# Kernel tuning notes

Measured on AMD Instinct MI355X. Metric: run time of the kernel, lower is better.

## Reference

```python
import jax, jax.numpy as jnp
import numpy as np
import math

B, S, D, H_HEADS, K_SPAN = 2, 2048, 64, 12, 512  # batch, seq, head dim, heads, pos_ebd_size


def setup_inputs() -> dict:
    key = jax.random.key(0)
    ks = jax.random.split(key, 12)
    init = lambda k, shp: (jax.random.normal(k, shp, dtype=jnp.float32) * 0.02)
    H = jax.random.normal(ks[0], (B, S, D), dtype=jnp.float32)
    pos_embeddings = jax.random.normal(ks[1], (2 * K_SPAN, D), dtype=jnp.float32)
    # classic DeBERTa relative positions: i - j (2-D, as required by the torch code path)
    idx = jnp.arange(S)
    relative_pos = (idx[:, None] - idx[None, :]).astype(jnp.int64)
    OH = H_HEADS * D
    return {
        "H": H,
        "pos_embeddings": pos_embeddings,
        "relative_pos": relative_pos,
        "Wq": init(ks[2], (OH, D)), "bq": jnp.zeros((OH,), jnp.float32),
        "Wk": init(ks[3], (OH, D)), "bk": jnp.zeros((OH,), jnp.float32),
        "Wv": init(ks[4], (OH, D)), "bv": jnp.zeros((OH,), jnp.float32),
        "Wpq": init(ks[5], (OH, D)), "bpq": jnp.zeros((OH,), jnp.float32),
        "Wpk": init(ks[6], (OH, D)), "bpk": jnp.zeros((OH,), jnp.float32),
    }


def _heads(x):
    # [..., S, h*d] -> [..., h, S, d]
    b, s, _ = x.shape
    return x.reshape(b, s, H_HEADS, D).transpose(0, 2, 1, 3)


def reference(H, pos_embeddings, relative_pos, Wq, bq, Wk, bk, Wv, bv, Wpq, bpq, Wpk, bpk):
    proj = lambda x, W, b: x @ W.T + b
    q = _heads(proj(H, Wq, bq))  # [B,h,S,d]
    k = _heads(proj(H, Wk, bk))
    v = _heads(proj(H, Wv, bv))

    # content-to-content scores
    scores = jnp.einsum('bhqd,bhkd->bhqk', q, k)  # [B,h,S,S]

    # relative position projections over the full 2K span
    pk = proj(pos_embeddings, Wpk, bpk).reshape(2 * K_SPAN, H_HEADS, D).transpose(1, 0, 2)  # [h,2K,d]
    pq = proj(pos_embeddings, Wpq, bpq).reshape(2 * K_SPAN, H_HEADS, D).transpose(1, 0, 2)

    rel = relative_pos.astype(jnp.int32)
    # content-to-position: gather over 2K axis with clamped (i-j)+K
    c2p = jnp.einsum('bhqd,hrd->bhqr', q, pk)  # [B,h,S,2K]
    c2p_pos = jnp.clip(rel + K_SPAN, 0, 2 * K_SPAN - 1)  # [S,S]
    c2p_idx = jnp.broadcast_to(c2p_pos[None, None], (B, H_HEADS, S, S))
    c2p_att = jnp.take_along_axis(c2p, c2p_idx, axis=-1)  # [B,h,S,S]

    # position-to-content: gather over 2K axis with clamped -(i-j)+K, then transpose
    p2c = jnp.einsum('bhkd,hrd->bhkr', k, pq)  # [B,h,S,2K]
    p2c_pos = jnp.clip(-rel + K_SPAN, 0, 2 * K_SPAN - 1)
    p2c_idx = jnp.broadcast_to(p2c_pos[None, None], (B, H_HEADS, S, S))
    p2c_att = jnp.take_along_axis(p2c, p2c_idx, axis=-1).swapaxes(-1, -2)  # [B,h,S,S]

    scores = (scores + c2p_att + p2c_att) / math.sqrt(D * 3)
    probs = jax.nn.softmax(scores, axis=-1)
    ctx = jnp.einsum('bhqk,bhkd->bhqd', probs, v)  # [B,h,S,d]
    return ctx.transpose(0, 2, 1, 3).reshape(B, S, H_HEADS * D)
```

## Files before the change

kernel.cpp:

```cpp
#include <hip/hip_runtime.h>
#include <math.h>


#define S_LEN 2048
#define NH    12
#define TWOK  1024
#define QSZ   3145728
#define PSZ   786432
#define POSF  11010048

typedef __bf16 bf16x8 __attribute__((ext_vector_type(8)));
typedef unsigned short u16x8 __attribute__((ext_vector_type(8)));
typedef unsigned short u16x4 __attribute__((ext_vector_type(4)));
typedef float f32x4  __attribute__((ext_vector_type(4)));
typedef float f32x16 __attribute__((ext_vector_type(16)));
typedef unsigned int u32x4 __attribute__((ext_vector_type(4)));

__device__ __forceinline__ unsigned short f2bf(float f) {
  return __builtin_bit_cast(unsigned short, (__bf16)f);
}
__device__ __forceinline__ unsigned pk2bf(float a, float b) {
  return ((unsigned)__builtin_bit_cast(unsigned short, (__bf16)b) << 16)
       | (unsigned)__builtin_bit_cast(unsigned short, (__bf16)a);
}
__device__ __forceinline__ float bf2f(unsigned short h) {
  return __builtin_bit_cast(float, ((unsigned)h) << 16);
}
__device__ __forceinline__ bf16x8 ld_bf8(const unsigned short* p) {
  return __builtin_bit_cast(bf16x8, *(const u16x8*)p);
}

__global__ __launch_bounds__(256) void prep_kernel(
    const float* __restrict__ Hx, const float* __restrict__ pos,
    const float* __restrict__ Wq, const float* __restrict__ Wk,
    const float* __restrict__ Wv, const float* __restrict__ Wpk,
    const float* __restrict__ Wpq,
    const float* __restrict__ bq, const float* __restrict__ bk,
    const float* __restrict__ bv, const float* __restrict__ bpk,
    const float* __restrict__ bpq,
    unsigned short* __restrict__ whi, unsigned short* __restrict__ wlo,
    unsigned short* __restrict__ wall, float* __restrict__ ball) {
  int t0 = blockIdx.x * 256 + threadIdx.x;
  for (int pass = 0; pass < 8; ++pass) {
    int idx = t0 + pass * 73728;
    if (idx < 327680) {
      float v = (idx < 262144) ? Hx[idx] : pos[idx - 262144];
      __bf16 hi = (__bf16)v;
      float lo = v - (float)hi;
      whi[idx] = __builtin_bit_cast(unsigned short, hi);
      wlo[idx] = f2bf(lo);
    } else if (idx < 573440) {
      int k = idx - 327680;
      int mat = k / 49152, off = k - mat * 49152;
      const float* W = mat==0?Wq: mat==1?Wk: mat==2?Wv: mat==3?Wpk:Wpq;
      wall[k] = f2bf(W[off]);
    } else if (idx < 577280) {
      int k = idx - 573440;
      int mat = k / 768, off = k - mat * 768;
      const float* B = mat==0?bq: mat==1?bk: mat==2?bv: mat==3?bpk:bpq;
      ball[k] = B[off];
    }
  }
}

__global__ __launch_bounds__(256) void proj_gemm(
    const unsigned short* __restrict__ whi, const unsigned short* __restrict__ wlo,
    const unsigned short* __restrict__ wall, const float* __restrict__ ball,
    unsigned short* __restrict__ ws) {
  unsigned short* qg  = ws;
  unsigned short* kg  = ws + QSZ;
  unsigned short* vtg = ws + 2 * QSZ;
  unsigned short* pkg = ws + 3 * QSZ;
  unsigned short* pqg = ws + 3 * QSZ + PSZ;

  int tid = threadIdx.x, w = tid >> 6, l = tid & 63, lg = l >> 4, lr = l & 15;

  for (int tt = 0; tt < 4; ++tt) {
    int tile = blockIdx.x * 4 + tt;
    int rbase, obase, wrow, isA;
    if (tile < 2304) { rbase = (tile / 36) * 64;        obase = (tile % 36) * 64; wrow = obase;        isA = 1; }
    else { int b2 = tile - 2304; rbase = 4096 + (b2 / 24) * 64; obase = (b2 % 24) * 64; wrow = 2304 + obase; isA = 0; }

    int mat = obase / 768;
    int h = (obase % 768) >> 6;
    int ohrow = wrow + w * 16;

    bf16x8 wf[2];
    #pragma unroll
    for (int ks = 0; ks < 2; ++ks)
      wf[ks] = ld_bf8(wall + (ohrow + lr) * 64 + ks * 32 + 8 * lg);

    if (isA && mat == 2) {
      float bias = ball[ohrow + lr];
      int d = w * 16 + lr;
      #pragma unroll
      for (int tg = 0; tg < 4; ++tg) {
        f32x4 acc = {0.f, 0.f, 0.f, 0.f};
        #pragma unroll
        for (int ks = 0; ks < 2; ++ks) {
          bf16x8 xh = ld_bf8(whi + (rbase + tg * 16 + lr) * 64 + ks * 32 + 8 * lg);
          bf16x8 xl = ld_bf8(wlo + (rbase + tg * 16 + lr) * 64 + ks * 32 + 8 * lg);
          acc = __builtin_amdgcn_mfma_f32_16x16x32_bf16(xh, wf[ks], acc, 0, 0, 0);
          acc = __builtin_amdgcn_mfma_f32_16x16x32_bf16(xl, wf[ks], acc, 0, 0, 0);
        }
        int tok0 = rbase + tg * 16 + 4 * lg;
        int bb = tok0 >> 11, i0 = tok0 & 2047, bh = bb * NH + h;
        u16x4 pv;
        #pragma unroll
        for (int e = 0; e < 4; ++e) pv[e] = f2bf(acc[e] + bias);
        *(u16x4*)(vtg + (size_t)(bh * 64 + d) * S_LEN + i0) = pv;
      }
    } else {
      float4 bias4 = *(const float4*)(ball + ohrow + 4 * lg);
      int d0 = w * 16 + 4 * lg;
      #pragma unroll
      for (int tg = 0; tg < 4; ++tg) {
        f32x4 acc = {0.f, 0.f, 0.f, 0.f};
        #pragma unroll
        for (int ks = 0; ks < 2; ++ks) {
          bf16x8 xh = ld_bf8(whi + (rbase + tg * 16 + lr) * 64 + ks * 32 + 8 * lg);
          bf16x8 xl = ld_bf8(wlo + (rbase + tg * 16 + lr) * 64 + ks * 32 + 8 * lg);
          acc = __builtin_amdgcn_mfma_f32_16x16x32_bf16(wf[ks], xh, acc, 0, 0, 0);
          acc = __builtin_amdgcn_mfma_f32_16x16x32_bf16(wf[ks], xl, acc, 0, 0, 0);
        }
        int tok = rbase + tg * 16 + lr;
        u16x4 pv;
        pv[0] = f2bf(acc[0] + bias4.x); pv[1] = f2bf(acc[1] + bias4.y);
        pv[2] = f2bf(acc[2] + bias4.z); pv[3] = f2bf(acc[3] + bias4.w);
        if (isA) {
          int bb = tok >> 11, i = tok & 2047, bh = bb * NH + h;
          unsigned short* dst = (mat == 0 ? qg : kg) + (size_t)(bh * S_LEN + i) * 64 + d0;
          *(u16x4*)dst = pv;
        } else {
          int prow = tok - 4096;
          unsigned short* dst = (mat == 0 ? pkg : pqg) + (size_t)(h * TWOK + prow) * 64 + d0;
          *(u16x4*)dst = pv;
        }
      }
    }
  }
}

__global__ __launch_bounds__(256) void pos_dots(
    const unsigned short* __restrict__ ws, float* __restrict__ c2p0,
    float* __restrict__ c2p1023, float* __restrict__ p2c0,
    float* __restrict__ p2c1023) {
  int t0 = blockIdx.x * 256 + threadIdx.x;
  for (int pass = 0; pass < 4; ++pass) {
    int t = t0 + pass * 24576;
    int isK = t >= 49152;
    int row = isK ? t - 49152 : t;
    int h = (row >> 11) % NH;
    const unsigned short* src = ws + (isK ? QSZ : 0) + row * 64;
    const unsigned short* pA = ws + 3 * QSZ + (isK ? PSZ : 0) + (h * TWOK) * 64;
    const unsigned short* pB = pA + 1023 * 64;
    float a0 = 0.f, a1 = 0.f;
    #pragma unroll
    for (int c = 0; c < 8; ++c) {
      u16x8 xv = *(const u16x8*)(src + c * 8);
      u16x8 av = *(const u16x8*)(pA + c * 8);
      u16x8 bv = *(const u16x8*)(pB + c * 8);
      #pragma unroll
      for (int e = 0; e < 8; ++e) {
        float x = bf2f(xv[e]);
        a0 += x * bf2f(av[e]);
        a1 += x * bf2f(bv[e]);
      }
    }
    if (isK) { p2c0[row] = a0; p2c1023[row] = a1; }
    else     { c2p0[row] = a0; c2p1023[row] = a1; }
  }
}

template<int SPLIT>
__global__ __launch_bounds__(512, 2) void attn_kernel(
    const unsigned short* __restrict__ ws, float* __restrict__ out,
    unsigned short* __restrict__ ctxP, float* __restrict__ mlP) {
  const unsigned short* qg  = ws;
  const unsigned short* kg  = ws + QSZ;
  const unsigned short* vtg = ws + 2 * QSZ;
  const unsigned short* pkg = ws + 3 * QSZ;
  const unsigned short* pqg = ws + 3 * QSZ + PSZ;
  const float* c2p0g    = (const float*)(ws + POSF);
  const float* c2p1023g = c2p0g + 49152;
  const float* p2c0g    = c2p0g + 98304;
  const float* p2c1023g = c2p0g + 147456;

  __shared__ __align__(16) unsigned int tbl2all[8 * 2048];
  unsigned int* tbl2 = tbl2all + (threadIdx.x >> 6) * 2048;

  const int bid = blockIdx.x;
  const int g = bid & 7;
  const int wid = threadIdx.x >> 6;
  const int u = (bid >> 3) * 8 + wid;
  const int sk = u & (SPLIT - 1);
  const int v = u / SPLIT;
  const int bh = 8 * (v % 3) + g;
  const int it32 = v / 3;
  const int b = bh / NH, h = bh - b * NH;
  const int l = threadIdx.x & 63;
  const int iL = l & 31, h5 = l >> 5;
  const int i0w = it32 * 32;
  const int ig = i0w + iL;

  const unsigned short* qb  = qg  + bh * (S_LEN * 64);
  const unsigned short* kb  = kg  + bh * (S_LEN * 64);
  const unsigned short* vb  = vtg + bh * (64 * S_LEN);
  const unsigned short* pkb = pkg + h * (TWOK * 64);
  const unsigned short* pqb = pqg + h * (TWOK * 64);

  const float CS = 1.4426950408889634f / sqrtf(192.0f);

  bf16x8 qf[4];
  #pragma unroll
  for (int kc = 0; kc < 4; ++kc)
    qf[kc] = ld_bf8(qb + ig * 64 + kc * 16 + 8 * h5);

  const float c2pLO = c2p0g[bh * S_LEN + ig];
  const float c2pHI = c2p1023g[bh * S_LEN + ig];

  f32x16 ctx0 = 0.f, ctx1 = 0.f;
  float m_ = -1e30f, l_ = 0.f;

  for (int t = 0; t < 32 / SPLIT; ++t) {
    const int jt = sk + t * SPLIT;
    const int j0 = jt * 64;
    const int D0w = 512 + i0w - j0;
    const int rlo = D0w - 63;
    const int rhi = rlo + 94;

    bf16x8 kf0[4], kf1[4];
    #pragma unroll
    for (int kc = 0; kc < 4; ++kc) {
      kf0[kc] = ld_bf8(kb + (j0 + iL) * 64 + kc * 16 + 8 * h5);
      kf1[kc] = ld_bf8(kb + (j0 + 32 + iL) * 64 + kc * 16 + 8 * h5);
    }
    bf16x8 vf0[4], vf1[4];
    #pragma unroll
    for (int kc = 0; kc < 4; ++kc) {
      vf0[kc] = ld_bf8(vb + (iL) * S_LEN + j0 + kc * 16 + 8 * h5);
      vf1[kc] = ld_bf8(vb + (32 + iL) * S_LEN + j0 + kc * 16 + 8 * h5);
    }

    f32x16 s0 = 0.f, s1 = 0.f;
    #pragma unroll
    for (int kc = 0; kc < 4; ++kc) {
      s0 = __builtin_amdgcn_mfma_f32_32x32x16_bf16(kf0[kc], qf[kc], s0, 0, 0, 0);
      s1 = __builtin_amdgcn_mfma_f32_32x32x16_bf16(kf1[kc], qf[kc], s1, 0, 0, 0);
    }

    if (rlo >= 1023) {
      float pa = p2c1023g[bh * S_LEN + j0 + iL];
      float pb = p2c1023g[bh * S_LEN + j0 + 32 + iL];
      #pragma unroll
      for (int rr = 0; rr < 16; ++rr) {
        const int j32 = (rr & 3) + 8 * (rr >> 2) + 4 * h5;
        s0[rr] = (s0[rr] + c2pHI + __shfl(pa, j32)) * CS;
        s1[rr] = (s1[rr] + c2pHI + __shfl(pb, j32)) * CS;
      }
    } else if (rhi <= 0) {
      float pa = p2c0g[bh * S_LEN + j0 + iL];
      float pb = p2c0g[bh * S_LEN + j0 + 32 + iL];
      #pragma unroll
      for (int rr = 0; rr < 16; ++rr) {
        const int j32 = (rr & 3) + 8 * (rr >> 2) + 4 * h5;
        s0[rr] = (s0[rr] + c2pLO + __shfl(pa, j32)) * CS;
        s1[rr] = (s1[rr] + c2pLO + __shfl(pb, j32)) * CS;
      }
    } else {
      const int rminc = rlo < 0 ? 0 : rlo;
      const int rmaxc = rhi > 1023 ? 1023 : rhi;
      const int bstart = rminc > 928 ? 928 : rminc;
      const int nbands = ((rmaxc - bstart) >> 5) + 1;
      const int base = D0w - bstart;
      const int interior = (rlo >= 0) & (rhi <= 1023);

      for (int nb = 0; nb < nbands; ++nb) {
        const int relb0 = nb * 32;
        const bool needC  = (relb0 <= base + 31) && (relb0 + 31 >= base - 63);
        const bool needP0 = (relb0 <= base + 31) && (relb0 + 31 >= base - 31);
        const bool needP1 = (relb0 <= base - 1)  && (relb0 + 31 >= base - 63);
        const int rrow = bstart + relb0 + iL;

        if (needC) {
          f32x16 ac = 0.f;
          #pragma unroll
          for (int kc = 0; kc < 4; ++kc) {
            bf16x8 fk = ld_bf8(pkb + rrow * 64 + kc * 16 + 8 * h5);
            ac = __builtin_amdgcn_mfma_f32_32x32x16_bf16(fk, qf[kc], ac, 0, 0, 0);
          }
          #pragma unroll
          for (int q4 = 0; q4 < 4; ++q4) {
            #pragma unroll
            for (int e = 0; e < 4; ++e) {
              const int relb = relb0 + 8 * q4 + 4 * h5 + e;
              const int js = base + iL - relb;
              if (js >= 0 && js < 64)
                ((unsigned short*)tbl2)[(js * 32 + iL) * 2] = f2bf(ac[4 * q4 + e]);
            }
          }
        }
        if (needP0 | needP1) {
          f32x16 a0 = 0.f, a1 = 0.f;
          #pragma unroll
          for (int kc = 0; kc < 4; ++kc) {
            bf16x8 fq = ld_bf8(pqb + rrow * 64 + kc * 16 + 8 * h5);
            if (needP0) a0 = __builtin_amdgcn_mfma_f32_32x32x16_bf16(fq, kf0[kc], a0, 0, 0, 0);
            if (needP1) a1 = __builtin_amdgcn_mfma_f32_32x32x16_bf16(fq, kf1[kc], a1, 0, 0, 0);
          }
          #pragma unroll
          for (int q4 = 0; q4 < 4; ++q4) {
            #pragma unroll
            for (int e = 0; e < 4; ++e) {
              const int relb = relb0 + 8 * q4 + 4 * h5 + e;
              if (needP0) {
                const int i2 = relb + iL - base;
                if (i2 >= 0 && i2 < 32)
                  ((unsigned short*)tbl2)[(iL * 32 + i2) * 2 + 1] = f2bf(a0[4 * q4 + e]);
              }
              if (needP1) {
                const int i2 = relb + 32 + iL - base;
                if (i2 >= 0 && i2 < 32)
                  ((unsigned short*)tbl2)[((32 + iL) * 32 + i2) * 2 + 1] = f2bf(a1[4 * q4 + e]);
              }
            }
          }
        }
      }
      asm volatile("s_waitcnt lgkmcnt(0)" ::: "memory");

      if (interior) {
        #pragma unroll
        for (int rr = 0; rr < 16; ++rr) {
          const int j32 = (rr & 3) + 8 * (rr >> 2) + 4 * h5;
          const unsigned t0 = tbl2[j32 * 32 + iL];
          const unsigned t1 = tbl2[(32 + j32) * 32 + iL];
          s0[rr] = (s0[rr] + bf2f((unsigned short)t0) + bf2f((unsigned short)(t0 >> 16))) * CS;
          s1[rr] = (s1[rr] + bf2f((unsigned short)t1) + bf2f((unsigned short)(t1 >> 16))) * CS;
        }
      } else {
        const int D0 = D0w + iL;
        float paL = p2c0g[bh * S_LEN + j0 + iL];
        float paH = p2c1023g[bh * S_LEN + j0 + iL];
        float pbL = p2c0g[bh * S_LEN + j0 + 32 + iL];
        float pbH = p2c1023g[bh * S_LEN + j0 + 32 + iL];
        #pragma unroll
        for (int rr = 0; rr < 16; ++rr) {
          const int j32 = (rr & 3) + 8 * (rr >> 2) + 4 * h5;
          const int raw0 = D0 - j32, raw1 = D0 - 32 - j32;
          const unsigned t0 = tbl2[j32 * 32 + iL];
          const unsigned t1 = tbl2[(32 + j32) * 32 + iL];
          const float saL = __shfl(paL, j32), saH = __shfl(paH, j32);
          const float sbL = __shfl(pbL, j32), sbH = __shfl(pbH, j32);
          float c0 = raw0 <= 0 ? c2pLO : (raw0 >= 1023 ? c2pHI : bf2f((unsigned short)t0));
          float p0 = raw0 <= 0 ? saL   : (raw0 >= 1023 ? saH   : bf2f((unsigned short)(t0 >> 16)));
          float c1 = raw1 <= 0 ? c2pLO : (raw1 >= 1023 ? c2pHI : bf2f((unsigned short)t1));
          float p1 = raw1 <= 0 ? sbL   : (raw1 >= 1023 ? sbH   : bf2f((unsigned short)(t1 >> 16)));
          s0[rr] = (s0[rr] + c0 + p0) * CS;
          s1[rr] = (s1[rr] + c1 + p1) * CS;
        }
      }
    }

    float vmax = s0[0];
    #pragma unroll
    for (int rr = 1; rr < 16; ++rr) vmax = fmaxf(vmax, s0[rr]);
    #pragma unroll
    for (int rr = 0; rr < 16; ++rr) vmax = fmaxf(vmax, s1[rr]);
    vmax = fmaxf(vmax, __shfl_xor(vmax, 32));
    float mx = fmaxf(m_, vmax);
    float fs = __builtin_amdgcn_exp2f(m_ - mx);
    m_ = mx;
    float sum = 0.f;
    #pragma unroll
    for (int rr = 0; rr < 16; ++rr) { s0[rr] = __builtin_amdgcn_exp2f(s0[rr] - mx); sum += s0[rr]; }
    #pragma unroll
    for (int rr = 0; rr < 16; ++rr) { s1[rr] = __builtin_amdgcn_exp2f(s1[rr] - mx); sum += s1[rr]; }
    sum += __shfl_xor(sum, 32);
    l_ = l_ * fs + sum;
    if (!__all(fs == 1.0f)) { ctx0 *= fs; ctx1 *= fs; }

    bf16x8 pf[4];
    #pragma unroll
    for (int kc = 0; kc < 4; ++kc) {
      const int c = kc & 1;
      const f32x16& sj = (kc >> 1) ? s1 : s0;
      unsigned X0 = pk2bf(sj[8*c+0], sj[8*c+1]);
      unsigned X1 = pk2bf(sj[8*c+2], sj[8*c+3]);
      unsigned Y0 = pk2bf(sj[8*c+4], sj[8*c+5]);
      unsigned Y1 = pk2bf(sj[8*c+6], sj[8*c+7]);
      unsigned sx0 = (unsigned)__shfl_xor((int)X0, 32);
      unsigned sx1 = (unsigned)__shfl_xor((int)X1, 32);
      unsigned sy0 = (unsigned)__shfl_xor((int)Y0, 32);
      unsigned sy1 = (unsigned)__shfl_xor((int)Y1, 32);
      u32x4 f;
      f[0] = h5 ? sy0 : X0;
      f[1] = h5 ? sy1 : X1;
      f[2] = h5 ? Y0 : sx0;
      f[3] = h5 ? Y1 : sx1;
      pf[kc] = __builtin_bit_cast(bf16x8, f);
    }

    #pragma unroll
    for (int kc = 0; kc < 4; ++kc) {
      ctx0 = __builtin_amdgcn_mfma_f32_32x32x16_bf16(vf0[kc], pf[kc], ctx0, 0, 0, 0);
      ctx1 = __builtin_amdgcn_mfma_f32_32x32x16_bf16(vf1[kc], pf[kc], ctx1, 0, 0, 0);
    }
  }

  if constexpr (SPLIT == 1) {
    float inv = 1.0f / l_;
    float* ob = out + (b * S_LEN + ig) * 768 + h * 64;
    #pragma unroll
    for (int q4 = 0; q4 < 4; ++q4) {
      float4 o0 = {ctx0[4*q4+0]*inv, ctx0[4*q4+1]*inv, ctx0[4*q4+2]*inv, ctx0[4*q4+3]*inv};
      *(float4*)(ob + 8 * q4 + 4 * h5) = o0;
      float4 o1 = {ctx1[4*q4+0]*inv, ctx1[4*q4+1]*inv, ctx1[4*q4+2]*inv, ctx1[4*q4+3]*inv};
      *(float4*)(ob + 32 + 8 * q4 + 4 * h5) = o1;
    }
  } else {
    const int rowg = ((bh * 64 + it32) * SPLIT + sk) * 32 + iL;
    unsigned short* cp = ctxP + (size_t)rowg * 64;
    #pragma unroll
    for (int q4 = 0; q4 < 4; ++q4) {
      u16x4 p0, p1;
      #pragma unroll
      for (int e = 0; e < 4; ++e) { p0[e] = f2bf(ctx0[4*q4+e]); p1[e] = f2bf(ctx1[4*q4+e]); }
      *(u16x4*)(cp + 8 * q4 + 4 * h5) = p0;
      *(u16x4*)(cp + 32 + 8 * q4 + 4 * h5) = p1;
    }
    ((float2*)mlP)[rowg] = make_float2(m_, l_);
  }
}

template<int SPLIT>
__global__ __launch_bounds__(256) void combine_kernel(
    const unsigned short* __restrict__ ctxP, const float* __restrict__ mlP,
    float* __restrict__ out) {
  int t0 = blockIdx.x * 256 + threadIdx.x;
  for (int pass = 0; pass < 4; ++pass) {
    int t = t0 + pass * 196608;
    int row = t >> 4, dc = t & 15;
    int bh = row >> 11, i = row & 2047;
    int it32 = i >> 5, iL = i & 31;
    int pbase = ((bh * 64 + it32) * SPLIT) * 32 + iL;
    float m[SPLIT], lv[SPLIT];
    float M = -1e30f;
    #pragma unroll
    for (int s = 0; s < SPLIT; ++s) {
      float2 ml = ((const float2*)mlP)[pbase + s * 32];
      m[s] = ml.x; lv[s] = ml.y;
      M = fmaxf(M, ml.x);
    }
    float L = 0.f, w[SPLIT];
    #pragma unroll
    for (int s = 0; s < SPLIT; ++s) { w[s] = exp2f(m[s] - M); L += lv[s] * w[s]; }
    float4 o = {0.f, 0.f, 0.f, 0.f};
    #pragma unroll
    for (int s = 0; s < SPLIT; ++s) {
      u16x4 c = *(const u16x4*)(ctxP + (size_t)(pbase + s * 32) * 64 + dc * 4);
      o.x += bf2f(c[0]) * w[s]; o.y += bf2f(c[1]) * w[s];
      o.z += bf2f(c[2]) * w[s]; o.w += bf2f(c[3]) * w[s];
    }
    float invL = 1.0f / L;
    int b = bh / NH, h = bh - b * NH;
    float* op = out + (size_t)(b * S_LEN + i) * 768 + h * 64 + dc * 4;
    *(float4*)op = make_float4(o.x * invL, o.y * invL, o.z * invL, o.w * invL);
  }
}

extern "C" void kernel_launch(void* const* d_in, const int* in_sizes, int n_in,
                              void* d_out, int out_size, void* d_ws, size_t ws_size,
                              hipStream_t stream) {
  (void)in_sizes; (void)n_in; (void)out_size;
  const float* Hx  = (const float*)d_in[0];
  const float* pos = (const float*)d_in[1];
  const float* Wq  = (const float*)d_in[3];  const float* bq  = (const float*)d_in[4];
  const float* Wk  = (const float*)d_in[5];  const float* bk  = (const float*)d_in[6];
  const float* Wv  = (const float*)d_in[7];  const float* bv  = (const float*)d_in[8];
  const float* Wpq = (const float*)d_in[9];  const float* bpq = (const float*)d_in[10];
  const float* Wpk = (const float*)d_in[11]; const float* bpk = (const float*)d_in[12];
  unsigned short* ws = (unsigned short*)d_ws;

  unsigned short* scratch = (unsigned short*)d_out;
  unsigned short* whi  = scratch;
  unsigned short* wlo  = scratch + 327680;
  unsigned short* wall = scratch + 655360;
  float*          ball = (float*)(scratch + 901120);

  float* c2p0g    = (float*)(ws + POSF);
  float* c2p1023g = c2p0g + 49152;
  float* p2c0g    = c2p0g + 98304;
  float* p2c1023g = c2p0g + 147456;

  const size_t base_u16 = POSF + 393216;
  const size_t unit_bytes = 6684672;
  int SPLIT = (ws_size >= base_u16 * 2 + 4 * unit_bytes) ? 4
            : (ws_size >= base_u16 * 2 + 2 * unit_bytes) ? 2 : 1;
  unsigned short* ctxP = ws + base_u16;
  float* mlP = (float*)(ctxP + (size_t)SPLIT * 3145728);

  prep_kernel<<<288, 256, 0, stream>>>(Hx, pos, Wq, Wk, Wv, Wpk, Wpq,
                                       bq, bk, bv, bpk, bpq, whi, wlo, wall, ball);
  proj_gemm<<<672, 256, 0, stream>>>(whi, wlo, wall, ball, ws);
  pos_dots<<<96, 256, 0, stream>>>(ws, c2p0g, c2p1023g, p2c0g, p2c1023g);

  float* outf = (float*)d_out;
  if (SPLIT == 4) {
    attn_kernel<4><<<768, 512, 0, stream>>>(ws, outf, ctxP, mlP);
    combine_kernel<4><<<768, 256, 0, stream>>>(ctxP, mlP, outf);
  } else if (SPLIT == 2) {
    attn_kernel<2><<<384, 512, 0, stream>>>(ws, outf, ctxP, mlP);
    combine_kernel<2><<<768, 256, 0, stream>>>(ctxP, mlP, outf);
  } else {
    attn_kernel<1><<<192, 512, 0, stream>>>(ws, outf, ctxP, mlP);
  }
}
```

Baseline: 344.5 us.

## Prefetch position-embedding band fragments and shrink attention blocks to four waves

Position-key and position-query band fragments are now loaded before the content QK MFMAs and double-buffered across bands (A/B/A), instead of being loaded inside each band's MFMA loop. V fragment loads are deferred until after the band work so they do not compete for registers with the prefetched data. Blocks shrink from 8 to 4 waves with launch bounds 256,1, so the grid doubles and shared memory per block halves. The aim is to hide global-load latency in the banded path. The cost is more live registers per wave, and the occupancy hint changes.

```diff
diff --git a/kernel.cpp b/kernel.cpp
--- a/kernel.cpp
+++ b/kernel.cpp
@@ -173,7 +173,7 @@
 }
 
 template<int SPLIT>
-__global__ __launch_bounds__(512, 2) void attn_kernel(
+__global__ __launch_bounds__(256, 1) void attn_kernel(
     const unsigned short* __restrict__ ws, float* __restrict__ out,
     unsigned short* __restrict__ ctxP, float* __restrict__ mlP) {
   const unsigned short* qg  = ws;
@@ -186,13 +186,13 @@
   const float* p2c0g    = c2p0g + 98304;
   const float* p2c1023g = c2p0g + 147456;
 
-  __shared__ __align__(16) unsigned int tbl2all[8 * 2048];
+  __shared__ __align__(16) unsigned int tbl2all[4 * 2048];
   unsigned int* tbl2 = tbl2all + (threadIdx.x >> 6) * 2048;
 
   const int bid = blockIdx.x;
   const int g = bid & 7;
   const int wid = threadIdx.x >> 6;
-  const int u = (bid >> 3) * 8 + wid;
+  const int u = (bid >> 3) * 4 + wid;
   const int sk = u & (SPLIT - 1);
   const int v = u / SPLIT;
   const int bh = 8 * (v % 3) + g;
@@ -228,6 +228,7 @@
     const int D0w = 512 + i0w - j0;
     const int rlo = D0w - 63;
     const int rhi = rlo + 94;
+    const bool banded = (rlo < 1023) && (rhi > 0);
 
     bf16x8 kf0[4], kf1[4];
     #pragma unroll
@@ -235,11 +236,32 @@
       kf0[kc] = ld_bf8(kb + (j0 + iL) * 64 + kc * 16 + 8 * h5);
       kf1[kc] = ld_bf8(kb + (j0 + 32 + iL) * 64 + kc * 16 + 8 * h5);
     }
-    bf16x8 vf0[4], vf1[4];
-    #pragma unroll
-    for (int kc = 0; kc < 4; ++kc) {
-      vf0[kc] = ld_bf8(vb + (iL) * S_LEN + j0 + kc * 16 + 8 * h5);
-      vf1[kc] = ld_bf8(vb + (32 + iL) * S_LEN + j0 + kc * 16 + 8 * h5);
+
+    int bstart = 0, nbands = 0, base = 0, interior = 0;
+    const unsigned short* pk0 = pkb;
+    const unsigned short* pq0 = pqb;
+    bf16x8 fkA[4], fqA[4], fkB[4], fqB[4];
+    if (banded) {
+      const int rminc = rlo < 0 ? 0 : rlo;
+      const int rmaxc = rhi > 1023 ? 1023 : rhi;
+      bstart = rminc > 928 ? 928 : rminc;
+      nbands = ((rmaxc - bstart) >> 5) + 1;
+      base = D0w - bstart;
+      interior = (rlo >= 0) & (rhi <= 1023);
+      pk0 = pkb + (bstart + iL) * 64 + 8 * h5;
+      pq0 = pqb + (bstart + iL) * 64 + 8 * h5;
+      #pragma unroll
+      for (int kc = 0; kc < 4; ++kc) {
+        fkA[kc] = ld_bf8(pk0 + kc * 16);
+        fqA[kc] = ld_bf8(pq0 + kc * 16);
+      }
+      if (nbands > 1) {
+        #pragma unroll
+        for (int kc = 0; kc < 4; ++kc) {
+          fkB[kc] = ld_bf8(pk0 + 2048 + kc * 16);
+          fqB[kc] = ld_bf8(pq0 + 2048 + kc * 16);
+        }
+      }
     }
 
     f32x16 s0 = 0.f, s1 = 0.f;
@@ -249,46 +271,35 @@
       s1 = __builtin_amdgcn_mfma_f32_32x32x16_bf16(kf1[kc], qf[kc], s1, 0, 0, 0);
     }
 
-    if (rlo >= 1023) {
-      float pa = p2c1023g[bh * S_LEN + j0 + iL];
-      float pb = p2c1023g[bh * S_LEN + j0 + 32 + iL];
+    bf16x8 vf0[4], vf1[4];
+
+    if (!banded) {
+      const float* pg = (rlo >= 1023) ? p2c1023g : p2c0g;
+      const float cA = (rlo >= 1023) ? c2pHI : c2pLO;
+      float pa = pg[bh * S_LEN + j0 + iL];
+      float pb = pg[bh * S_LEN + j0 + 32 + iL];
+      #pragma unroll
+      for (int kc = 0; kc < 4; ++kc) {
+        vf0[kc] = ld_bf8(vb + (iL) * S_LEN + j0 + kc * 16 + 8 * h5);
+        vf1[kc] = ld_bf8(vb + (32 + iL) * S_LEN + j0 + kc * 16 + 8 * h5);
+      }
       #pragma unroll
       for (int rr = 0; rr < 16; ++rr) {
         const int j32 = (rr & 3) + 8 * (rr >> 2) + 4 * h5;
-        s0[rr] = (s0[rr] + c2pHI + __shfl(pa, j32)) * CS;
-        s1[rr] = (s1[rr] + c2pHI + __shfl(pb, j32)) * CS;
-      }
-    } else if (rhi <= 0) {
-      float pa = p2c0g[bh * S_LEN + j0 + iL];
-      float pb = p2c0g[bh * S_LEN + j0 + 32 + iL];
-      #pragma unroll
-      for (int rr = 0; rr < 16; ++rr) {
-        const int j32 = (rr & 3) + 8 * (rr >> 2) + 4 * h5;
-        s0[rr] = (s0[rr] + c2pLO + __shfl(pa, j32)) * CS;
-        s1[rr] = (s1[rr] + c2pLO + __shfl(pb, j32)) * CS;
+        s0[rr] = (s0[rr] + cA + __shfl(pa, j32)) * CS;
+        s1[rr] = (s1[rr] + cA + __shfl(pb, j32)) * CS;
       }
     } else {
-      const int rminc = rlo < 0 ? 0 : rlo;
-      const int rmaxc = rhi > 1023 ? 1023 : rhi;
-      const int bstart = rminc > 928 ? 928 : rminc;
-      const int nbands = ((rmaxc - bstart) >> 5) + 1;
-      const int base = D0w - bstart;
-      const int interior = (rlo >= 0) & (rhi <= 1023);
-
-      for (int nb = 0; nb < nbands; ++nb) {
+      auto bandwork = [&](int nb, const bf16x8* fk, const bf16x8* fq) {
         const int relb0 = nb * 32;
         const bool needC  = (relb0 <= base + 31) && (relb0 + 31 >= base - 63);
         const bool needP0 = (relb0 <= base + 31) && (relb0 + 31 >= base - 31);
         const bool needP1 = (relb0 <= base - 1)  && (relb0 + 31 >= base - 63);
-        const int rrow = bstart + relb0 + iL;
-
         if (needC) {
           f32x16 ac = 0.f;
           #pragma unroll
-          for (int kc = 0; kc < 4; ++kc) {
-            bf16x8 fk = ld_bf8(pkb + rrow * 64 + kc * 16 + 8 * h5);
-            ac = __builtin_amdgcn_mfma_f32_32x32x16_bf16(fk, qf[kc], ac, 0, 0, 0);
-          }
+          for (int kc = 0; kc < 4; ++kc)
+            ac = __builtin_amdgcn_mfma_f32_32x32x16_bf16(fk[kc], qf[kc], ac, 0, 0, 0);
           #pragma unroll
           for (int q4 = 0; q4 < 4; ++q4) {
             #pragma unroll
@@ -304,9 +315,8 @@
           f32x16 a0 = 0.f, a1 = 0.f;
           #pragma unroll
           for (int kc = 0; kc < 4; ++kc) {
-            bf16x8 fq = ld_bf8(pqb + rrow * 64 + kc * 16 + 8 * h5);
-            if (needP0) a0 = __builtin_amdgcn_mfma_f32_32x32x16_bf16(fq, kf0[kc], a0, 0, 0, 0);
-            if (needP1) a1 = __builtin_amdgcn_mfma_f32_32x32x16_bf16(fq, kf1[kc], a1, 0, 0, 0);
+            if (needP0) a0 = __builtin_amdgcn_mfma_f32_32x32x16_bf16(fq[kc], kf0[kc], a0, 0, 0, 0);
+            if (needP1) a1 = __builtin_amdgcn_mfma_f32_32x32x16_bf16(fq[kc], kf1[kc], a1, 0, 0, 0);
           }
           #pragma unroll
           for (int q4 = 0; q4 < 4; ++q4) {
@@ -326,6 +336,23 @@
             }
           }
         }
+      };
+
+      bandwork(0, fkA, fqA);
+      if (nbands > 2) {
+        #pragma unroll
+        for (int kc = 0; kc < 4; ++kc) {
+          fkA[kc] = ld_bf8(pk0 + 4096 + kc * 16);
+          fqA[kc] = ld_bf8(pq0 + 4096 + kc * 16);
+        }
+      }
+      if (nbands > 1) bandwork(1, fkB, fqB);
+      if (nbands > 2) bandwork(2, fkA, fqA);
+
+      #pragma unroll
+      for (int kc = 0; kc < 4; ++kc) {
+        vf0[kc] = ld_bf8(vb + (iL) * S_LEN + j0 + kc * 16 + 8 * h5);
+        vf1[kc] = ld_bf8(vb + (32 + iL) * S_LEN + j0 + kc * 16 + 8 * h5);
       }
       asm volatile("s_waitcnt lgkmcnt(0)" ::: "memory");
 
@@ -507,12 +534,12 @@
 
   float* outf = (float*)d_out;
   if (SPLIT == 4) {
-    attn_kernel<4><<<768, 512, 0, stream>>>(ws, outf, ctxP, mlP);
+    attn_kernel<4><<<1536, 256, 0, stream>>>(ws, outf, ctxP, mlP);
     combine_kernel<4><<<768, 256, 0, stream>>>(ctxP, mlP, outf);
   } else if (SPLIT == 2) {
-    attn_kernel<2><<<384, 512, 0, stream>>>(ws, outf, ctxP, mlP);
+    attn_kernel<2><<<768, 256, 0, stream>>>(ws, outf, ctxP, mlP);
     combine_kernel<2><<<768, 256, 0, stream>>>(ctxP, mlP, outf);
   } else {
-    attn_kernel<1><<<192, 512, 0, stream>>>(ws, outf, ctxP, mlP);
-  }
-}
+    attn_kernel<1><<<384, 256, 0, stream>>>(ws, outf, ctxP, mlP);
+  }
+}
```

New measurement: 376.4 us. 1.09x slower.
